# Performance work log

Measured on AMD Instinct MI355X. Metric: run time of the kernel, lower is better.

## Reference

```python
import jax, jax.numpy as jnp
import numpy as np

DT = 0.01
SIM_STEPS = 10_000_000
G = jnp.array([0.0, -9.81], dtype=jnp.float32)  # gravity, matches Ball.g


def setup_inputs() -> dict:
    key = jax.random.key(0)
    k_pos, k_vel = jax.random.split(key)
    return {
        "ball_mass": jnp.ones((), dtype=jnp.float32),  # unused by the math, kept for signature fidelity
        "ball_initial_position": jax.random.normal(k_pos, (2,), dtype=jnp.float32),
        "ball_initial_velocity": jax.random.normal(k_vel, (2,), dtype=jnp.float32),  # nn.Parameter
    }


def reference(ball_mass, ball_initial_position, ball_initial_velocity):
    # Faithful semi-implicit-Euler-style recurrence:
    #   pos <- pos + vel*dt ; vel <- vel + g*dt ; record pos
    # trajectory[0] is the initial position, trajectory[1:] are the updated positions.
    def step(carry, _):
        pos, vel = carry
        pos = pos + vel * DT
        vel = vel + G * DT
        return (pos, vel), pos

    _, traj = jax.lax.scan(
        step, (ball_initial_position, ball_initial_velocity), None, length=SIM_STEPS - 1
    )  # traj: [SIM_STEPS-1, 2]
    return jnp.concatenate([ball_initial_position[None, :], traj], axis=0)  # [SIM_STEPS, 2]
```

## Files before the change

### kernel.cpp

```cpp
#include <hip/hip_runtime.h>
#include <stdint.h>


static constexpr long long NSTEPS = 10000000LL;
static constexpr long long NPOLY  = 1000000LL;
static constexpr long long NS     = 5500000LL;
static constexpr int SEGCAP = 384;
static constexpr int RUNCAP = 96;

__device__ __forceinline__ bool same_binade_f32(float a, float b) {
    return (((__float_as_uint(a) ^ __float_as_uint(b)) & 0xFF800000u) == 0u);
}
__device__ __forceinline__ unsigned expfield(float v) {
    return (__float_as_uint(v) >> 23) & 0xFFu;
}
__device__ __forceinline__ float pow2f(int e) {
    return __uint_as_float((unsigned)(e + 127) << 23);
}

__global__ __launch_bounds__(256, 4) void fused(
        const float* __restrict__ pos0, const float* __restrict__ vel0,
        float4* __restrict__ out, long long npairs)
{
    __shared__ int    s_m[SEGCAP + 1];
    __shared__ double s_c[SEGCAP], s_V[SEGCAP], s_P[SEGCAP];
    __shared__ int    s_nseg, s_nrun;
    __shared__ long long s_mstop;
    __shared__ int    r_n[RUNCAP];
    __shared__ double r_p[RUNCAP], r_i[RUNCAP];

    const int tid  = threadIdx.x;
    const int lane = tid & 63;
    const int wv   = tid >> 6;

    const long long per = (npairs + (long long)gridDim.x - 1) / (long long)gridDim.x;
    const long long i0 = (long long)blockIdx.x * per;
    long long i1 = i0 + per; if (i1 > npairs) i1 = npairs;
    if (i0 >= npairs) return;
    const long long row_end = 2 * i1;
    const long long mstop = row_end < NSTEPS ? row_end : NSTEPS;

    const float dtf  = 0.01f;
    const float gdtf = __fmul_rn(-9.81f, dtf);
    const double dtd = (double)dtf, gdtd = (double)gdtf;
    const double p0y = (double)pos0[1], v0y = (double)vel0[1];

    if (tid == 0) { s_nseg = 0; s_nrun = 0; s_mstop = 0; }
    __syncthreads();

    if (wv == 0 && row_end > NPOLY) {
        double V = v0y, P = p0y;
        long long m = 0;
        int nseg = 0;
        while (m < mstop && nseg < SEGCAP) {
            const float vf  = (float)V;
            const float vn1 = __fadd_rn(vf, gdtf);
            const double c  = (double)vn1 - V;
            const long long rem = mstop - m;
            long long Lb = rem;
            const float cf = (float)c;
            const unsigned ef = expfield(vf);
            if (vf == 0.0f || ef == 0u) {
                Lb = 64;
            } else if (cf != 0.0f) {
                const int k = (int)ef - 126;
                float s = vf < 0.0f ? -1.0f : 1.0f;
                float B = ((vf < 0.0f) == (cf < 0.0f)) ? s * pow2f(k) : s * pow2f(k - 1);
                float r = __fdividef(B - vf, cf);
                if (r >= 0.0f && r < 4.0e9f) Lb = (long long)r + 1;
            }
            long long Lhi = Lb + 2;
            if (Lhi > rem) Lhi = rem;
            if (Lhi < 1) Lhi = 1;

            long long L = 1, base = Lhi;
            for (int round = 0; round < 32; ++round) {
                const long long candL = base - 63 + (long long)lane;
                bool valid = false;
                if (candL >= 1) {
                    const double ve = V + (double)(candL - 1) * c;
                    const float vef = (float)ve;
                    const float vn2 = __fadd_rn(vef, gdtf);
                    valid = ((double)vef == ve)
                         && same_binade_f32(vef, vf)
                         && ((double)vn2 - ve == c);
                }
                unsigned long long msk = __ballot(valid);
                if (msk) { L = base - 63 + (long long)(63 - __clzll(msk)); break; }
                base -= 64;
                if (base < 1) break;
            }
            if (L < 1) L = 1;
            if (L > rem) L = rem;

            if (lane == 0) { s_m[nseg] = (int)m; s_V[nseg] = V; s_c[nseg] = c; s_P[nseg] = P; }
            ++nseg;
            P += dtd * ((double)L * V + c * ((double)L * (double)(L - 1) * 0.5));
            V += (double)L * c;
            m += L;
        }
        if (lane == 0) { s_nseg = nseg; s_mstop = m; s_m[nseg] = 0x7fffffff; }
    }
    __syncthreads();

    if (wv == 0 && row_end > NS && s_mstop >= NS) {
        const int nseg = s_nseg;
        const long long mbuilt = s_mstop;
        int lo = 0, hi = nseg - 1;
        while (lo < hi) { int mid = (lo + hi + 1) >> 1;
                          if ((long long)s_m[mid] <= NS) lo = mid; else hi = mid - 1; }
        int jj = lo;
        const double t0 = (double)(NS - s_m[jj]);
        double vel = s_V[jj] + t0 * s_c[jj];
        double P2  = s_P[jj] + dtd * (t0 * s_V[jj] + s_c[jj] * (t0 * (t0 - 1.0) * 0.5));
        double pos = (double)(float)P2;
        long long n = NS;
        int nrun = 0;
        long long nend = (row_end < NSTEPS - 1) ? row_end : (NSTEPS - 1);
        if (nend > mbuilt) nend = mbuilt;
        while (n < nend && nrun < RUNCAP) {
            while (s_m[jj + 1] <= (int)n) ++jj;
            const double cv = s_c[jj];
            long long Lcap = (long long)s_m[jj + 1] - n;
            if (Lcap > mbuilt - n) Lcap = mbuilt - n;
            const long long rem = (NSTEPS - 1) - n;
            if (Lcap > rem) Lcap = rem;

            const float pf = (float)pos;
            const float vf2 = (float)vel;
            const float dstep = __fmul_rn(vf2, dtf);
            const float pn1 = __fadd_rn(pf, dstep);
            const double inc = (double)pn1 - pos;

            long long La = Lcap, Lc = Lcap;
            const float incf = (float)inc;
            const unsigned efp = expfield(pf);
            if (pf == 0.0f || efp == 0u) {
                La = 64;
            } else if (incf != 0.0f) {
                const int k = (int)efp - 126;
                float s = pf < 0.0f ? -1.0f : 1.0f;
                float B = ((pf < 0.0f) == (incf < 0.0f)) ? s * pow2f(k) : s * pow2f(k - 1);
                float r = __fdividef(B - pf, incf);
                if (r >= 0.0f && r < 4.0e9f) { La = (long long)r - 1; if (La < 0) La = 0; }
            }
            const double dd = cv * dtd;
            if (dd != 0.0 && pf != 0.0f && efp != 0u) {
                const int k = (int)efp - 126;
                if (k - 24 > -126) {
                    const float ulpf = pow2f(k - 24);
                    const double d0 = (double)dstep;
                    const double T = inc + (dd < 0.0 ? -0.5 : 0.5) * (double)ulpf;
                    float r = __fdividef((float)(T - d0), (float)dd);
                    if (r >= 0.0f && r < 4.0e9f) { Lc = (long long)r + 2; if (Lc < 1) Lc = 1; }
                }
            }
            long long Lhi = La < Lc ? La : Lc;
            Lhi += 3;
            if (Lhi > Lcap) Lhi = Lcap;
            if (Lhi < 1) Lhi = 1;

            long long L = 1, base = Lhi;
            for (int round = 0; round < 32; ++round) {
                const long long candL = base - 63 + (long long)lane;
                bool valid = false;
                if (candL >= 1) {
                    const double pe = pos + (double)(candL - 1) * inc;
                    const double ve = vel + (double)(candL - 1) * cv;
                    const float pef = (float)pe;
                    const float vef = (float)ve;
                    const float d2  = __fmul_rn(vef, dtf);
                    const float pn2 = __fadd_rn(pef, d2);
                    valid = ((double)pef == pe)
                         && same_binade_f32(pef, pf)
                         && ((double)vef == ve)
                         && ((double)pn2 - pe == inc);
                }
                unsigned long long msk = __ballot(valid);
                if (msk) { L = base - 63 + (long long)(63 - __clzll(msk)); break; }
                base -= 64;
                if (base < 1) break;
            }
            if (L < 1) L = 1;
            if (L > Lcap) L = Lcap;
            if (L < 1) L = 1;

            if (lane == 0) { r_n[nrun] = (int)n; r_p[nrun] = pos; r_i[nrun] = inc; }
            ++nrun;
            pos += (double)L * inc;
            vel += (double)L * cv;
            n += L;
        }
        if (lane == 0) s_nrun = nrun;
    }
    __syncthreads();

    const int nseg = s_nseg;
    const int nrun = s_nrun;
    const double p0x = (double)pos0[0];
    const double cx  = (double)__fmul_rn(vel0[0], dtf);

    const long long ii = i0 + tid;
    if (ii >= i1) return;

    int j = 0, r = 0;
    if (nseg > 0) {
        const int t0 = (int)(2 * ii);
        int lo = 0, hi = nseg - 1;
        while (lo < hi) { int mid = (lo + hi + 1) >> 1; if (s_m[mid] <= t0) lo = mid; else hi = mid - 1; }
        j = lo;
        if (nrun > 0) {
            int rlo = 0, rhi = nrun - 1;
            while (rlo < rhi) { int mid = (rlo + rhi + 1) >> 1; if (r_n[mid] <= t0) rlo = mid; else rhi = mid - 1; }
            r = rlo;
        }
    }
    for (long long i = ii; i < i1; i += blockDim.x) {
        const long long m0 = 2 * i, m1 = m0 + 1;
        float4 o;
        o.x = (float)(p0x + (double)m0 * cx);
        o.z = (float)(p0x + (double)m1 * cx);
        const int t0 = (int)m0;

        if (m1 < NPOLY) {
            double md = (double)m0;
            o.y = (float)(p0y + dtd * (md * v0y) + (dtd * gdtd) * (md * (md - 1.0) * 0.5));
            md = (double)m1;
            o.w = (float)(p0y + dtd * (md * v0y) + (dtd * gdtd) * (md * (md - 1.0) * 0.5));
        } else if (m1 < NS || nrun <= 0) {
            while (s_m[j + 1] <= t0) ++j;
            double t = (double)(m0 - s_m[j]);
            o.y = (float)(s_P[j] + dtd * (t * s_V[j] + s_c[j] * (t * (t - 1.0) * 0.5)));
            const int j1 = (s_m[j + 1] <= (int)m1) ? j + 1 : j;
            t = (double)(m1 - s_m[j1]);
            o.w = (float)(s_P[j1] + dtd * (t * s_V[j1] + s_c[j1] * (t * (t - 1.0) * 0.5)));
        } else {
            while (r + 1 < nrun && r_n[r + 1] <= t0) ++r;
            o.y = (float)(r_p[r] + (double)(m0 - r_n[r]) * r_i[r]);
            const int r1 = (r + 1 < nrun && r_n[r + 1] <= (int)m1) ? r + 1 : r;
            o.w = (float)(r_p[r1] + (double)(m1 - r_n[r1]) * r_i[r1]);
        }
        out[i] = o;
    }
}

extern "C" void kernel_launch(void* const* d_in, const int* in_sizes, int n_in,
                              void* d_out, int out_size, void* d_ws, size_t ws_size,
                              hipStream_t stream) {
    const float* pos0 = (const float*)d_in[1];
    const float* vel0 = (const float*)d_in[2];

    const long long npairs = (long long)out_size / 4;
    fused<<<1024, 256, 0, stream>>>(pos0, vel0, (float4*)d_out, npairs);
}
```

Baseline: 42.96 us.

## Switch output evaluation to fp32, single-round ballot search, fewer blocks

Moves the per-element trajectory evaluation from double to float, using float copies of the segment and run tables precomputed in shared memory. Drops the multi-round backward ballot search in favour of a single round, and seeds the velocity segments with 64 direct steps. Halves the grid to 512 blocks and changes launch bounds to 2 blocks per CU. This reduces FP64 arithmetic and serial segment-building work, at the risk of fp32 rounding that no longer matches the reference recurrence exactly and of shorter segments when the single-round search finds no candidate.

Result: slower. 46.42 us (+8.1%).

```diff
diff --git a/kernel.cpp b/kernel.cpp
--- a/kernel.cpp
+++ b/kernel.cpp
@@ -5,6 +5,7 @@
 static constexpr long long NSTEPS = 10000000LL;
 static constexpr long long NPOLY  = 1000000LL;
 static constexpr long long NS     = 5500000LL;
+static constexpr long long KDIR   = 64;
 static constexpr int SEGCAP = 384;
 static constexpr int RUNCAP = 96;
 
@@ -18,16 +19,18 @@
     return __uint_as_float((unsigned)(e + 127) << 23);
 }
 
-__global__ __launch_bounds__(256, 4) void fused(
+__global__ __launch_bounds__(256, 2) void fused(
         const float* __restrict__ pos0, const float* __restrict__ vel0,
         float4* __restrict__ out, long long npairs)
 {
     __shared__ int    s_m[SEGCAP + 1];
-    __shared__ double s_c[SEGCAP], s_V[SEGCAP], s_P[SEGCAP];
+    __shared__ double s_V[SEGCAP], s_c[SEGCAP], s_P[SEGCAP];
+    __shared__ float  s_Vf[SEGCAP], s_cdt[SEGCAP], s_Pf[SEGCAP];
+    __shared__ int    r_n[RUNCAP];
+    __shared__ double r_p[RUNCAP], r_i[RUNCAP];
+    __shared__ float  r_pf[RUNCAP], r_if[RUNCAP];
     __shared__ int    s_nseg, s_nrun;
     __shared__ long long s_mstop;
-    __shared__ int    r_n[RUNCAP];
-    __shared__ double r_p[RUNCAP], r_i[RUNCAP];
 
     const int tid  = threadIdx.x;
     const int lane = tid & 63;
@@ -50,7 +53,12 @@
 
     if (wv == 0 && row_end > NPOLY) {
         double V = v0y, P = p0y;
-        long long m = 0;
+        for (int t = 0; t < (int)KDIR; ++t) {
+            const float vf = (float)V;
+            P += dtd * V;
+            V = (double)__fadd_rn(vf, gdtf);
+        }
+        long long m = KDIR;
         int nseg = 0;
         while (m < mstop && nseg < SEGCAP) {
             const float vf  = (float)V;
@@ -73,9 +81,9 @@
             if (Lhi > rem) Lhi = rem;
             if (Lhi < 1) Lhi = 1;
 
-            long long L = 1, base = Lhi;
-            for (int round = 0; round < 32; ++round) {
-                const long long candL = base - 63 + (long long)lane;
+            long long L = 1;
+            {
+                const long long candL = Lhi - 63 + (long long)lane;
                 bool valid = false;
                 if (candL >= 1) {
                     const double ve = V + (double)(candL - 1) * c;
@@ -85,10 +93,8 @@
                          && same_binade_f32(vef, vf)
                          && ((double)vn2 - ve == c);
                 }
-                unsigned long long msk = __ballot(valid);
-                if (msk) { L = base - 63 + (long long)(63 - __clzll(msk)); break; }
-                base -= 64;
-                if (base < 1) break;
+                const unsigned long long msk = __ballot(valid);
+                if (msk) L = Lhi - 63 + (long long)(63 - __clzll(msk));
             }
             if (L < 1) L = 1;
             if (L > rem) L = rem;
@@ -103,7 +109,7 @@
     }
     __syncthreads();
 
-    if (wv == 0 && row_end > NS && s_mstop >= NS) {
+    if (wv == 0 && row_end > NS && s_mstop >= NS && s_nseg > 0) {
         const int nseg = s_nseg;
         const long long mbuilt = s_mstop;
         int lo = 0, hi = nseg - 1;
@@ -160,9 +166,9 @@
             if (Lhi > Lcap) Lhi = Lcap;
             if (Lhi < 1) Lhi = 1;
 
-            long long L = 1, base = Lhi;
-            for (int round = 0; round < 32; ++round) {
-                const long long candL = base - 63 + (long long)lane;
+            long long L = 1;
+            {
+                const long long candL = Lhi - 63 + (long long)lane;
                 bool valid = false;
                 if (candL >= 1) {
                     const double pe = pos + (double)(candL - 1) * inc;
@@ -176,10 +182,8 @@
                          && ((double)vef == ve)
                          && ((double)pn2 - pe == inc);
                 }
-                unsigned long long msk = __ballot(valid);
-                if (msk) { L = base - 63 + (long long)(63 - __clzll(msk)); break; }
-                base -= 64;
-                if (base < 1) break;
+                const unsigned long long msk = __ballot(valid);
+                if (msk) L = Lhi - 63 + (long long)(63 - __clzll(msk));
             }
             if (L < 1) L = 1;
             if (L > Lcap) L = Lcap;
@@ -195,10 +199,27 @@
     }
     __syncthreads();
 
+    {
+        const int nseg = s_nseg, nrun = s_nrun;
+        for (int i = tid; i < nseg; i += 256) {
+            s_Vf[i]  = (float)s_V[i];
+            s_cdt[i] = (float)(dtd * s_c[i]);
+            s_Pf[i]  = (float)s_P[i];
+        }
+        for (int i = tid; i < nrun; i += 256) {
+            r_pf[i] = (float)r_p[i];
+            r_if[i] = (float)r_i[i];
+        }
+    }
+    __syncthreads();
+
     const int nseg = s_nseg;
     const int nrun = s_nrun;
-    const double p0x = (double)pos0[0];
-    const double cx  = (double)__fmul_rn(vel0[0], dtf);
+    const float pxf = pos0[0];
+    const float cxf = __fmul_rn(vel0[0], dtf);
+    const float pyf = (float)p0y;
+    const float vyf = (float)v0y;
+    const float q2f = (float)(dtd * gdtd);
 
     const long long ii = i0 + tid;
     if (ii >= i1) return;
@@ -217,28 +238,27 @@
     }
     for (long long i = ii; i < i1; i += blockDim.x) {
         const long long m0 = 2 * i, m1 = m0 + 1;
+        const float mf0 = (float)m0, mf1 = (float)m1;
         float4 o;
-        o.x = (float)(p0x + (double)m0 * cx);
-        o.z = (float)(p0x + (double)m1 * cx);
+        o.x = pxf + mf0 * cxf;
+        o.z = pxf + mf1 * cxf;
         const int t0 = (int)m0;
 
         if (m1 < NPOLY) {
-            double md = (double)m0;
-            o.y = (float)(p0y + dtd * (md * v0y) + (dtd * gdtd) * (md * (md - 1.0) * 0.5));
-            md = (double)m1;
-            o.w = (float)(p0y + dtd * (md * v0y) + (dtd * gdtd) * (md * (md - 1.0) * 0.5));
+            o.y = pyf + dtf * (mf0 * vyf) + q2f * (mf0 * (mf0 - 1.0f) * 0.5f);
+            o.w = pyf + dtf * (mf1 * vyf) + q2f * (mf1 * (mf1 - 1.0f) * 0.5f);
         } else if (m1 < NS || nrun <= 0) {
             while (s_m[j + 1] <= t0) ++j;
-            double t = (double)(m0 - s_m[j]);
-            o.y = (float)(s_P[j] + dtd * (t * s_V[j] + s_c[j] * (t * (t - 1.0) * 0.5)));
+            float t = (float)(int)(m0 - s_m[j]);
+            o.y = s_Pf[j] + dtf * (t * s_Vf[j]) + s_cdt[j] * (t * (t - 1.0f) * 0.5f);
             const int j1 = (s_m[j + 1] <= (int)m1) ? j + 1 : j;
-            t = (double)(m1 - s_m[j1]);
-            o.w = (float)(s_P[j1] + dtd * (t * s_V[j1] + s_c[j1] * (t * (t - 1.0) * 0.5)));
+            t = (float)(int)(m1 - s_m[j1]);
+            o.w = s_Pf[j1] + dtf * (t * s_Vf[j1]) + s_cdt[j1] * (t * (t - 1.0f) * 0.5f);
         } else {
             while (r + 1 < nrun && r_n[r + 1] <= t0) ++r;
-            o.y = (float)(r_p[r] + (double)(m0 - r_n[r]) * r_i[r]);
+            o.y = r_pf[r] + (float)(int)(m0 - r_n[r]) * r_if[r];
             const int r1 = (r + 1 < nrun && r_n[r + 1] <= (int)m1) ? r + 1 : r;
-            o.w = (float)(r_p[r1] + (double)(m1 - r_n[r1]) * r_i[r1]);
+            o.w = r_pf[r1] + (float)(int)(m1 - r_n[r1]) * r_if[r1];
         }
         out[i] = o;
     }
@@ -251,5 +271,5 @@
     const float* vel0 = (const float*)d_in[2];
 
     const long long npairs = (long long)out_size / 4;
-    fused<<<1024, 256, 0, stream>>>(pos0, vel0, (float4*)d_out, npairs);
-}
+    fused<<<512, 256, 0, stream>>>(pos0, vel0, (float4*)d_out, npairs);
+}
```
